# Optimization experiments

Hardware: AMD Instinct MI355X
Metric: run time of the kernel (lower is better)

## Reference

```python
import jax, jax.numpy as jnp
import numpy as np


def setup_inputs() -> dict:
    key = jax.random.key(0)
    k1, k2, k3 = jax.random.split(key, 3)
    B, S, E = 2, 2048, 2048
    H, O, A = 16, 1024, 128  # heads, codebook options, head_size (E = H*A)
    x = jax.random.normal(k1, (B, S, E), dtype=jnp.float32)
    vq_head_weights = jax.random.normal(k2, (H, O, A), dtype=jnp.float32) * 0.02
    vq_codebooks = jax.random.normal(k3, (H, O, A), dtype=jnp.float32) * 0.02
    temperature = jnp.ones((1,), dtype=jnp.float32)
    return {"x": x, "vq_head_weights": vq_head_weights, "vq_codebooks": vq_codebooks, "temperature": temperature}


def reference(x, vq_head_weights, vq_codebooks, temperature):
    # Training-mode, frozen, use_temperature=True path (straight-through VQ):
    # probs = one_hot(argmax(logits)) + softmax(logits/T) - stop_grad(softmax(logits/T))
    B, S, E = x.shape
    H, O, A = vq_head_weights.shape
    x_prepped = x.reshape(B, S, H, A)
    logits = jnp.einsum('bsha,hoa->bsho', x_prepped, vq_head_weights)
    probs = jax.nn.softmax(logits / temperature[0], axis=-1)
    argmax = jnp.argmax(logits, axis=-1)  # [B,S,H]
    hard_probs = jax.nn.one_hot(argmax, O, dtype=logits.dtype)
    probs = hard_probs + probs - jax.lax.stop_gradient(probs)
    out = jnp.einsum('bsho,hoa->bsha', probs, vq_codebooks)
    return out.reshape(B, S, E)
```

## Files before the change

### kernel.cpp

```cpp
#include <hip/hip_runtime.h>

typedef _Float16 half8 __attribute__((ext_vector_type(8)));
typedef float    f32x16 __attribute__((ext_vector_type(16)));

constexpr int kH = 16;
constexpr int kO = 1024;
constexpr int kA = 128;
constexpr int kBS = 4096;
constexpr int MTILE = 256;
constexpr int NITER = 16;
constexpr int NBUF = 4;

typedef const __attribute__((address_space(1))) uint32_t* gas_ptr;
typedef __attribute__((address_space(3))) uint32_t* las_ptr;

__global__ void split_w(const float* __restrict__ w, ushort* __restrict__ wp) {
    const int lane = threadIdx.x & 63;
    const int gw   = blockIdx.x * 4 + (threadIdx.x >> 6);
    const int ks   = lane >> 3;
    const int half = (lane >> 2) & 1;
    const int j    = (2 * lane) & 7;
#pragma unroll
    for (int q = 0; q < 4; ++q) {
        int r = gw * 4 + q;
        int h = r >> 10, o = r & 1023, t = o >> 5, o31 = o & 31;
        float2 v = *(const float2*)(w + r * kA + lane * 2);
        _Float16 h0 = (_Float16)v.x, h1 = (_Float16)v.y;
        _Float16 l0 = (_Float16)(v.x - (float)h0), l1 = (_Float16)(v.y - (float)h1);
        ushort2 hv = { __builtin_bit_cast(ushort, h0), __builtin_bit_cast(ushort, h1) };
        ushort2 lv = { __builtin_bit_cast(ushort, l0), __builtin_bit_cast(ushort, l1) };
        ushort* d = wp + (h * 32 + t) * 8192 + ks * 512 + (half * 32 + o31) * 8 + j;
        *(ushort2*)d = hv;
        *(ushort2*)(d + 4096) = lv;
    }
}

#define PHASE_SYNC(N) do {                                        \
    asm volatile("s_waitcnt vmcnt(" #N ")" ::: "memory");         \
    __builtin_amdgcn_s_barrier();                                 \
    asm volatile("" ::: "memory");                                \
  } while (0)

__launch_bounds__(512, 2)
__global__ void vq_argmax_gather(const float* __restrict__ x,
                                 const ushort* __restrict__ wp,
                                 const float* __restrict__ cb,
                                 float* __restrict__ out) {
    __shared__ ushort wtile[NBUF][2][8192];
    __shared__ float red_max[2][MTILE];
    __shared__ int   red_idx[2][MTILE];

    const int tid   = threadIdx.x;
    const int lane  = tid & 63;
    const int wv    = tid >> 6;
    const int nhalf = wv >> 2;
    const int msub  = wv & 3;
    const int bid   = blockIdx.x;
    const int h  = ((bid & 7) << 1) | ((bid >> 3) & 1);
    const int p0 = (bid >> 4) * MTILE;

    const int l31  = lane & 31;
    const int half = lane >> 5;

    const ushort* wh_base = wp + h * 32 * 8192;

    auto stage = [&](int it, int buf) {
#pragma unroll
        for (int q = 0; q < 4; ++q) {
            int c   = wv * 4 + q;
            int nh  = c >> 4, rem = c & 15;
            const ushort* g = wh_base + (nh * 16 + it) * 8192 + rem * 512 + lane * 8;
            ushort* l = &wtile[buf][nh][rem * 512];
            __builtin_amdgcn_global_load_lds((gas_ptr)(const void*)g,
                                             (las_ptr)(void*)l, 16, 0, 0);
        }
    };

    stage(0, 0); stage(1, 1); stage(2, 2);
    asm volatile("" ::: "memory");

    const int mrow0 = p0 + msub * 64 + l31;
    const float* xb0 = x + (mrow0 * kH + h) * kA + half * 8;
    const float* xb1 = xb0 + 32 * kH * kA;
    half8 xh0[8], xl0[8], xh1[8], xl1[8];
    auto cvt8 = [&](const float* p, half8& hi, half8& lo) {
        float4 v0 = *(const float4*)(p);
        float4 v1 = *(const float4*)(p + 4);
        float va[8] = { v0.x, v0.y, v0.z, v0.w, v1.x, v1.y, v1.z, v1.w };
#pragma unroll
        for (int j = 0; j < 8; ++j) {
            _Float16 hj = (_Float16)va[j];
            hi[j] = hj;
            lo[j] = (_Float16)(va[j] - (float)hj);
        }
    };
#pragma unroll
    for (int ks = 0; ks < 8; ++ks) {
        cvt8(xb0 + ks * 16, xh0[ks], xl0[ks]);
        cvt8(xb1 + ks * 16, xh1[ks], xl1[ks]);
    }

    float best0 = -1e30f, best1 = -1e30f;
    int   bidx0 = 0,      bidx1 = 0;
    const int nwb = nhalf * (kO / 2);

    auto compute = [&](int it) {
        const int buf = it & 3;
        const ushort* lbase = &wtile[buf][nhalf][lane * 8];
        f32x16 acc0 = {}, acc1 = {};
        __builtin_amdgcn_s_setprio(1);
#pragma unroll
        for (int ks = 0; ks < 8; ++ks) {
            half8 wh = *(const half8*)(lbase + ks * 512);
            acc0 = __builtin_amdgcn_mfma_f32_32x32x16_f16(wh, xh0[ks], acc0, 0, 0, 0);
            acc1 = __builtin_amdgcn_mfma_f32_32x32x16_f16(wh, xh1[ks], acc1, 0, 0, 0);
        }
#pragma unroll
        for (int ks = 0; ks < 8; ++ks) {
            half8 wh = *(const half8*)(lbase + ks * 512);
            acc0 = __builtin_amdgcn_mfma_f32_32x32x16_f16(wh, xl0[ks], acc0, 0, 0, 0);
            acc1 = __builtin_amdgcn_mfma_f32_32x32x16_f16(wh, xl1[ks], acc1, 0, 0, 0);
        }
#pragma unroll
        for (int ks = 0; ks < 8; ++ks) {
            half8 wl = *(const half8*)(lbase + 4096 + ks * 512);
            acc0 = __builtin_amdgcn_mfma_f32_32x32x16_f16(wl, xh0[ks], acc0, 0, 0, 0);
            acc1 = __builtin_amdgcn_mfma_f32_32x32x16_f16(wl, xh1[ks], acc1, 0, 0, 0);
        }
        __builtin_amdgcn_s_setprio(0);

        float lv0 = acc0[0]; int lr0 = 0;
#pragma unroll
        for (int r = 1; r < 16; ++r)
            if (acc0[r] > lv0) { lv0 = acc0[r]; lr0 = r; }
        int li0 = nwb + it * 32 + 4 * half + (lr0 & 3) + 8 * (lr0 >> 2);
        if (lv0 > best0) { best0 = lv0; bidx0 = li0; }

        float lv1 = acc1[0]; int lr1 = 0;
#pragma unroll
        for (int r = 1; r < 16; ++r)
            if (acc1[r] > lv1) { lv1 = acc1[r]; lr1 = r; }
        int li1 = nwb + it * 32 + 4 * half + (lr1 & 3) + 8 * (lr1 >> 2);
        if (lv1 > best1) { best1 = lv1; bidx1 = li1; }
    };

    for (int it = 0; it < NITER - 3; ++it) {
        PHASE_SYNC(8);
        stage(it + 3, (it + 3) & 3);
        compute(it);
    }
    PHASE_SYNC(8); compute(NITER - 3);
    PHASE_SYNC(4); compute(NITER - 2);
    PHASE_SYNC(0); compute(NITER - 1);

    {
        float om = __shfl_xor(best0, 32, 64);
        int   oi = __shfl_xor(bidx0, 32, 64);
        if (om > best0 || (om == best0 && oi < bidx0)) { best0 = om; bidx0 = oi; }
        om = __shfl_xor(best1, 32, 64);
        oi = __shfl_xor(bidx1, 32, 64);
        if (om > best1 || (om == best1 && oi < bidx1)) { best1 = om; bidx1 = oi; }
    }
    if (half == 0) {
        red_max[nhalf][msub * 64 + l31]      = best0;
        red_idx[nhalf][msub * 64 + l31]      = bidx0;
        red_max[nhalf][msub * 64 + 32 + l31] = best1;
        red_idx[nhalf][msub * 64 + 32 + l31] = bidx1;
    }
    __syncthreads();

    for (int i = tid; i < MTILE * 32; i += 512) {
        int row = i >> 5, ch = i & 31;
        float m0 = red_max[0][row], m1 = red_max[1][row];
        int o = (m1 > m0) ? red_idx[1][row] : red_idx[0][row];
        float4 v = *(const float4*)(cb + (h * kO + o) * kA + ch * 4);
        *(float4*)(out + ((p0 + row) * kH + h) * kA + ch * 4) = v;
    }
}

extern "C" void kernel_launch(void* const* d_in, const int* in_sizes, int n_in,
                              void* d_out, int out_size, void* d_ws, size_t ws_size,
                              hipStream_t stream) {
    const float* x  = (const float*)d_in[0];
    const float* w  = (const float*)d_in[1];
    const float* cb = (const float*)d_in[2];
    float* out = (float*)d_out;

    ushort* wpacked = (ushort*)d_ws;

    split_w<<<dim3(1024), dim3(256), 0, stream>>>(w, wpacked);
    vq_argmax_gather<<<dim3((kBS / MTILE) * kH), dim3(512), 0, stream>>>(x, wpacked, cb, out);
}
```

Before: 148.9 us.

## Load packed weight fragments directly from global into registers, drop LDS staging

Replaces the 4-buffer LDS pipeline (global_load_lds with vmcnt-gated barriers) with direct per-lane global loads of the packed fp16 hi/lo weight fragments into registers. The hi fragment for the next tile is prefetched during the current tile's MFMAs. This removes the LDS traffic and the large shared allocation, which may allow higher occupancy. In exchange, each wave in the same N-half now reads the same weights from global/L2 four times instead of once per block, and latency hiding relies on a short register prefetch plus the extra register pressure.

```diff
diff --git a/kernel.cpp b/kernel.cpp
--- a/kernel.cpp
+++ b/kernel.cpp
@@ -9,10 +9,6 @@
 constexpr int kBS = 4096;
 constexpr int MTILE = 256;
 constexpr int NITER = 16;
-constexpr int NBUF = 4;
-
-typedef const __attribute__((address_space(1))) uint32_t* gas_ptr;
-typedef __attribute__((address_space(3))) uint32_t* las_ptr;
 
 __global__ void split_w(const float* __restrict__ w, ushort* __restrict__ wp) {
     const int lane = threadIdx.x & 63;
@@ -35,18 +31,11 @@
     }
 }
 
-#define PHASE_SYNC(N) do {                                        \
-    asm volatile("s_waitcnt vmcnt(" #N ")" ::: "memory");         \
-    __builtin_amdgcn_s_barrier();                                 \
-    asm volatile("" ::: "memory");                                \
-  } while (0)
-
 __launch_bounds__(512, 2)
 __global__ void vq_argmax_gather(const float* __restrict__ x,
                                  const ushort* __restrict__ wp,
                                  const float* __restrict__ cb,
                                  float* __restrict__ out) {
-    __shared__ ushort wtile[NBUF][2][8192];
     __shared__ float red_max[2][MTILE];
     __shared__ int   red_idx[2][MTILE];
 
@@ -62,22 +51,7 @@
     const int l31  = lane & 31;
     const int half = lane >> 5;
 
-    const ushort* wh_base = wp + h * 32 * 8192;
-
-    auto stage = [&](int it, int buf) {
-#pragma unroll
-        for (int q = 0; q < 4; ++q) {
-            int c   = wv * 4 + q;
-            int nh  = c >> 4, rem = c & 15;
-            const ushort* g = wh_base + (nh * 16 + it) * 8192 + rem * 512 + lane * 8;
-            ushort* l = &wtile[buf][nh][rem * 512];
-            __builtin_amdgcn_global_load_lds((gas_ptr)(const void*)g,
-                                             (las_ptr)(void*)l, 16, 0, 0);
-        }
-    };
-
-    stage(0, 0); stage(1, 1); stage(2, 2);
-    asm volatile("" ::: "memory");
+    const ushort* wb = wp + (h * 32 + nhalf * 16) * 8192 + lane * 8;
 
     const int mrow0 = p0 + msub * 64 + l31;
     const float* xb0 = x + (mrow0 * kH + h) * kA + half * 8;
@@ -100,34 +74,45 @@
         cvt8(xb1 + ks * 16, xh1[ks], xl1[ks]);
     }
 
+    half8 A[8], Bf[8];
+#pragma unroll
+    for (int ks = 0; ks < 8; ++ks)
+        A[ks] = *(const half8*)(wb + ks * 512);
+
     float best0 = -1e30f, best1 = -1e30f;
     int   bidx0 = 0,      bidx1 = 0;
     const int nwb = nhalf * (kO / 2);
 
-    auto compute = [&](int it) {
-        const int buf = it & 3;
-        const ushort* lbase = &wtile[buf][nhalf][lane * 8];
+    for (int it = 0; it < NITER; ++it) {
+        __builtin_amdgcn_s_barrier();
+        const ushort* tb = wb + it * 8192;
+
+#pragma unroll
+        for (int ks = 0; ks < 8; ++ks)
+            Bf[ks] = *(const half8*)(tb + 4096 + ks * 512);
+
         f32x16 acc0 = {}, acc1 = {};
-        __builtin_amdgcn_s_setprio(1);
 #pragma unroll
         for (int ks = 0; ks < 8; ++ks) {
-            half8 wh = *(const half8*)(lbase + ks * 512);
-            acc0 = __builtin_amdgcn_mfma_f32_32x32x16_f16(wh, xh0[ks], acc0, 0, 0, 0);
-            acc1 = __builtin_amdgcn_mfma_f32_32x32x16_f16(wh, xh1[ks], acc1, 0, 0, 0);
+            acc0 = __builtin_amdgcn_mfma_f32_32x32x16_f16(A[ks], xh0[ks], acc0, 0, 0, 0);
+            acc1 = __builtin_amdgcn_mfma_f32_32x32x16_f16(A[ks], xh1[ks], acc1, 0, 0, 0);
         }
 #pragma unroll
         for (int ks = 0; ks < 8; ++ks) {
-            half8 wh = *(const half8*)(lbase + ks * 512);
-            acc0 = __builtin_amdgcn_mfma_f32_32x32x16_f16(wh, xl0[ks], acc0, 0, 0, 0);
-            acc1 = __builtin_amdgcn_mfma_f32_32x32x16_f16(wh, xl1[ks], acc1, 0, 0, 0);
+            acc0 = __builtin_amdgcn_mfma_f32_32x32x16_f16(A[ks], xl0[ks], acc0, 0, 0, 0);
+            acc1 = __builtin_amdgcn_mfma_f32_32x32x16_f16(A[ks], xl1[ks], acc1, 0, 0, 0);
+        }
+        if (it + 1 < NITER) {
+            const ushort* nb = wb + (it + 1) * 8192;
+#pragma unroll
+            for (int ks = 0; ks < 8; ++ks)
+                A[ks] = *(const half8*)(nb + ks * 512);
         }
 #pragma unroll
         for (int ks = 0; ks < 8; ++ks) {
-            half8 wl = *(const half8*)(lbase + 4096 + ks * 512);
-            acc0 = __builtin_amdgcn_mfma_f32_32x32x16_f16(wl, xh0[ks], acc0, 0, 0, 0);
-            acc1 = __builtin_amdgcn_mfma_f32_32x32x16_f16(wl, xh1[ks], acc1, 0, 0, 0);
+            acc0 = __builtin_amdgcn_mfma_f32_32x32x16_f16(Bf[ks], xh0[ks], acc0, 0, 0, 0);
+            acc1 = __builtin_amdgcn_mfma_f32_32x32x16_f16(Bf[ks], xh1[ks], acc1, 0, 0, 0);
         }
-        __builtin_amdgcn_s_setprio(0);
 
         float lv0 = acc0[0]; int lr0 = 0;
 #pragma unroll
@@ -142,16 +127,7 @@
             if (acc1[r] > lv1) { lv1 = acc1[r]; lr1 = r; }
         int li1 = nwb + it * 32 + 4 * half + (lr1 & 3) + 8 * (lr1 >> 2);
         if (lv1 > best1) { best1 = lv1; bidx1 = li1; }
-    };
-
-    for (int it = 0; it < NITER - 3; ++it) {
-        PHASE_SYNC(8);
-        stage(it + 3, (it + 3) & 3);
-        compute(it);
     }
-    PHASE_SYNC(8); compute(NITER - 3);
-    PHASE_SYNC(4); compute(NITER - 2);
-    PHASE_SYNC(0); compute(NITER - 1);
 
     {
         float om = __shfl_xor(best0, 32, 64);
```

Result: slower. 152.2 us (+2.3%).
